# Kernel optimization log

Measured on AMD Instinct MI355X. Metric: run time of the kernel, lower is better.

Reference implementation:

```python
import jax, jax.numpy as jnp
import numpy as np

LOC_SIZE, CID_SIZE, UID_SIZE, TIM_SIZE = 10000, 300, 1000, 48
LOC_EMB, CID_EMB, UID_EMB, TIM_EMB = 256, 64, 64, 32
HID, ENC_HID = 500, 250            # hidden_size, history_hidden_size
SEQ, TGT = 2048, 256
INPUT = LOC_EMB + TIM_EMB + CID_EMB  # 352


def setup_inputs() -> dict:
    key = jax.random.key(0)
    ks = jax.random.split(key, 32)
    n = lambda i, shape, s=0.05: (jax.random.normal(ks[i], shape, dtype=jnp.float32) * s)
    d = {}
    d["loc"] = jax.random.randint(ks[0], (SEQ, 1), 0, LOC_SIZE)
    d["tim"] = jax.random.randint(ks[1], (SEQ, 1), 0, TIM_SIZE)
    d["cid"] = jax.random.randint(ks[2], (SEQ, 1), 0, CID_SIZE)
    d["uid"] = jax.random.randint(ks[3], (1,), 0, UID_SIZE)
    d["target"] = jax.random.randint(ks[4], (TGT, 1), 0, LOC_SIZE)
    d["target_len"] = TGT
    d["time_sim_matrix"] = jax.random.uniform(ks[5], (TIM_SIZE, TIM_SIZE), dtype=jnp.float32)
    # keep distances away from 0 since the model computes 1/dist
    d["poi_distance_matrix"] = jax.random.uniform(ks[6], (LOC_SIZE, LOC_SIZE), dtype=jnp.float32, minval=0.1, maxval=2.0)
    d["poi_cid_tim"] = jax.random.uniform(ks[7], (TIM_SIZE, CID_SIZE), dtype=jnp.float32)
    # embedding tables (emb_loc/emb_cid are pretrained+frozen in the original)
    d["weight"] = n(8, (LOC_SIZE, LOC_EMB))
    d["weight_cid"] = n(9, (CID_SIZE, CID_EMB))
    d["emb_uid_w"] = n(10, (UID_SIZE, UID_EMB))
    d["emb_tim_w"] = n(11, (TIM_SIZE, TIM_EMB))
    # bidirectional encoder LSTM (hidden 250), gate order i,f,g,o like torch
    d["enc_Wih_f"] = n(12, (4 * ENC_HID, INPUT))
    d["enc_Whh_f"] = n(13, (4 * ENC_HID, ENC_HID))
    d["enc_b_f"] = jnp.zeros((4 * ENC_HID,), jnp.float32)
    d["enc_Wih_b"] = n(14, (4 * ENC_HID, INPUT))
    d["enc_Whh_b"] = n(15, (4 * ENC_HID, ENC_HID))
    d["enc_b_b"] = jnp.zeros((4 * ENC_HID,), jnp.float32)
    # decoder LSTM (hidden 500)
    d["dec_Wih"] = n(16, (4 * HID, INPUT))
    d["dec_Whh"] = n(17, (4 * HID, HID))
    d["dec_b"] = jnp.zeros((4 * HID,), jnp.float32)
    # linear layers
    d["fc_user_w"] = n(18, (HID, UID_EMB))
    d["fc_user_b"] = jnp.zeros((HID,), jnp.float32)
    d["fc_final_w"] = n(19, (LOC_SIZE, 3 * HID))
    d["fc_final_b"] = jnp.zeros((LOC_SIZE,), jnp.float32)
    d["fc_final2_w"] = n(20, (HID, 3 * HID))
    d["fc_final2_b"] = jnp.zeros((HID,), jnp.float32)
    return d


def _lstm(x, Wih, Whh, b, H):
    """Single-layer LSTM, batch=1. x: [T, D] -> hs: [T, H]."""
    h0 = jnp.zeros((H,), x.dtype)
    c0 = jnp.zeros((H,), x.dtype)

    def step(carry, xt):
        h, c = carry
        z = Wih @ xt + Whh @ h + b
        i, f, g, o = jnp.split(z, 4)
        c = jax.nn.sigmoid(f) * c + jax.nn.sigmoid(i) * jnp.tanh(g)
        h = jax.nn.sigmoid(o) * jnp.tanh(c)
        return (h, c), h

    _, hs = jax.lax.scan(step, (h0, c0), x)
    return hs


def _table_attn(history, current, table, invert=False, causal=False):
    """Vectorized replacement for the nested-loop lookup attention.
    energies[i, j] = table[current[i], history[j]] (or its reciprocal),
    upper triangle left at 0 for the self-attn variants (as in the original),
    then softmax over the full row (torch F.softmax default dim=1 on 2D)."""
    e = table[current[:, None], history[None, :]]
    if invert:
        e = 1.0 / e
    if causal:
        nn_ = e.shape[0]
        e = jnp.where(jnp.tril(jnp.ones((nn_, nn_), bool)), e, jnp.zeros((), e.dtype))
    return jax.nn.softmax(e, axis=-1)


def reference(loc, tim, cid, uid, target, target_len,
              time_sim_matrix, poi_distance_matrix, poi_cid_tim,
              weight, weight_cid, emb_uid_w, emb_tim_w,
              enc_Wih_f, enc_Whh_f, enc_b_f, enc_Wih_b, enc_Whh_b, enc_b_b,
              dec_Wih, dec_Whh, dec_b,
              fc_user_w, fc_user_b, fc_final_w, fc_final_b, fc_final2_w, fc_final2_b):
    T = int(target_len)
    loc_f, tim_f, cid_f = loc[:, 0], tim[:, 0], cid[:, 0]

    # cross attention: current window attends to history via lookup tables
    attn_cid_time = _table_attn(cid_f[:-T], tim_f[-T:], poi_cid_tim)
    attn_loc = _table_attn(loc_f[:-T], loc_f[-T:], poi_distance_matrix, invert=True)
    attn_time = _table_attn(tim_f[:-T], tim_f[-T:], time_sim_matrix)
    # self attention on the current window (lower-triangular fill)
    self_cid_time = _table_attn(cid_f[-T:], tim_f[-T:], poi_cid_tim, causal=True)
    self_loc = _table_attn(loc_f[-T:], loc_f[-T:], poi_distance_matrix, invert=True, causal=True)
    self_time = _table_attn(tim_f[-T:], tim_f[-T:], time_sim_matrix, causal=True)

    # embeddings (dropout is identity in eval)
    x = jnp.concatenate([weight[loc_f], emb_tim_w[tim_f], weight_cid[cid_f]], axis=1)  # [SEQ, INPUT]
    hist_x, tgt_x = x[:-T], x[-T:]

    # bidirectional encoder over history
    hf = _lstm(hist_x, enc_Wih_f, enc_Whh_f, enc_b_f, ENC_HID)
    hb = _lstm(hist_x[::-1], enc_Wih_b, enc_Whh_b, enc_b_b, ENC_HID)[::-1]
    hidden_history = jnp.concatenate([hf, hb], axis=1)  # [SEQ-T, 2*ENC_HID=500]

    # decoder over current window
    hidden_state = _lstm(tgt_x, dec_Wih, dec_Whh, dec_b, HID)  # [T, 500]

    target_emb = weight[target[:, 0]]  # [T, LOC_EMB]

    uid_emb = emb_uid_w[uid] @ fc_user_w.T + fc_user_b  # [1, 500]
    user_attn = jax.nn.softmax(uid_emb @ hidden_history.T, axis=-1)  # [1, hist]
    context_user = user_attn @ hidden_history  # [1, 500]

    context = (attn_loc + attn_time + attn_cid_time) @ hidden_history  # [T, 500]
    hidden_state = (self_loc + self_time + self_cid_time) @ hidden_state  # [T, 500]

    hidden_state_all = hidden_state + uid_emb  # broadcast of repeat
    out = jnp.concatenate([hidden_state_all, context,
                           jnp.broadcast_to(context_user, (T, HID))], axis=1)  # [T, 1500]
    y = out @ fc_final_w.T + fc_final_b    # [T, LOC_SIZE]
    y1 = out @ fc_final2_w.T + fc_final2_b  # [T, HID]
    score = jax.nn.log_softmax(y, axis=-1)
    return score, y1, target_emb
```

## Files before the change

kernel.cpp:

```cpp
#include <hip/hip_runtime.h>
#include <stdint.h>

#define HIST 1792
#define TGT 256
#define SEQ 2048
#define INPUT 352
#define EHID 250
#define HID 500

typedef _Float16 h2_t __attribute__((ext_vector_type(2)));

static __device__ __forceinline__ float fdot2(uint32_t a, uint32_t b, float c) {
  return __builtin_amdgcn_fdot2(__builtin_bit_cast(h2_t, a),
                                __builtin_bit_cast(h2_t, b), c, false);
}
static __device__ __forceinline__ uint32_t packh2(float lo, float hi) {
  h2_t h; h[0] = (_Float16)lo; h[1] = (_Float16)hi;
  return __builtin_bit_cast(uint32_t, h);
}
static __device__ __forceinline__ uint4 packq(const float* p) {
  uint4 r;
  r.x = packh2(p[0], p[1]); r.y = packh2(p[2], p[3]);
  r.z = packh2(p[4], p[5]); r.w = packh2(p[6], p[7]);
  return r;
}
static __device__ __forceinline__ float dotq(uint4 w, uint4 h, float acc) {
  acc = fdot2(w.x, h.x, acc); acc = fdot2(w.y, h.y, acc);
  acc = fdot2(w.z, h.z, acc); acc = fdot2(w.w, h.w, acc);
  return acc;
}
static __device__ __forceinline__ float sigf(float x) {
  x = fminf(fmaxf(x, -30.f), 30.f);
  return 1.f / (1.f + __expf(-x));
}
static __device__ __forceinline__ float tanh_f(float x) {
  x = fminf(fmaxf(x, -15.f), 15.f);
  float e = __expf(2.f * x);
  return (e - 1.f) / (e + 1.f);
}

__global__ void k_embed(const int* __restrict__ loc, const int* __restrict__ tim,
                        const int* __restrict__ cid, const int* __restrict__ target,
                        const float* __restrict__ weight, const float* __restrict__ emb_tim_w,
                        const float* __restrict__ weight_cid,
                        float* __restrict__ x, float* __restrict__ te) {
  int t = blockIdx.x, tid = threadIdx.x;
  if (t < SEQ) {
    int l = loc[t], tm = tim[t], cd = cid[t];
    float* xr = x + (size_t)t * INPUT;
    for (int k = tid; k < 256; k += blockDim.x) xr[k] = weight[(size_t)l * 256 + k];
    for (int k = tid; k < 32; k += blockDim.x)  xr[256 + k] = emb_tim_w[tm * 32 + k];
    for (int k = tid; k < 64; k += blockDim.x)  xr[288 + k] = weight_cid[cd * 64 + k];
  } else {
    int i = t - SEQ;
    int tg = target[i];
    for (int k = tid; k < 256; k += blockDim.x) te[(size_t)i * 256 + k] = weight[(size_t)tg * 256 + k];
  }
}

__global__ void k_gemm_t(const float* __restrict__ A, int lda,
                         const float* __restrict__ W, const float* __restrict__ bias,
                         float* __restrict__ C, int ldc,
                         int M, int N, int K, int revA) {
  __shared__ float As[16][65];
  __shared__ float Ws[16][65];
  const int bn = blockIdx.x * 64, bm = blockIdx.y * 64;
  const int tid = threadIdx.x;
  const int tx = tid & 15, ty = tid >> 4;
  float acc[4][4] = {};
  for (int k0 = 0; k0 < K; k0 += 16) {
    for (int i = tid; i < 1024; i += 256) {
      int m = i >> 4, k = i & 15;
      int gm = bm + m, gk = k0 + k;
      float v = 0.f;
      if (gm < M && gk < K) { int am = revA ? (M - 1 - gm) : gm; v = A[(size_t)am * lda + gk]; }
      As[k][m] = v;
    }
    for (int i = tid; i < 1024; i += 256) {
      int n = i >> 4, k = i & 15;
      int gn = bn + n, gk = k0 + k;
      float v = 0.f;
      if (gn < N && gk < K) v = W[(size_t)gn * K + gk];
      Ws[k][n] = v;
    }
    __syncthreads();
#pragma unroll
    for (int k = 0; k < 16; k++) {
      float a0 = As[k][ty * 4 + 0], a1 = As[k][ty * 4 + 1], a2 = As[k][ty * 4 + 2], a3 = As[k][ty * 4 + 3];
      float b0 = Ws[k][tx * 4 + 0], b1 = Ws[k][tx * 4 + 1], b2 = Ws[k][tx * 4 + 2], b3 = Ws[k][tx * 4 + 3];
      acc[0][0] += a0 * b0; acc[0][1] += a0 * b1; acc[0][2] += a0 * b2; acc[0][3] += a0 * b3;
      acc[1][0] += a1 * b0; acc[1][1] += a1 * b1; acc[1][2] += a1 * b2; acc[1][3] += a1 * b3;
      acc[2][0] += a2 * b0; acc[2][1] += a2 * b1; acc[2][2] += a2 * b2; acc[2][3] += a2 * b3;
      acc[3][0] += a3 * b0; acc[3][1] += a3 * b1; acc[3][2] += a3 * b2; acc[3][3] += a3 * b3;
    }
    __syncthreads();
  }
  for (int i = 0; i < 4; i++) {
    int gm = bm + ty * 4 + i; if (gm >= M) continue;
    for (int j = 0; j < 4; j++) {
      int gn = bn + tx * 4 + j; if (gn >= N) continue;
      C[(size_t)gm * ldc + gn] = acc[i][j] + (bias ? bias[gn] : 0.f);
    }
  }
}

__global__ void k_gemm_nn(const float* __restrict__ A, int lda,
                          const float* __restrict__ B, int ldb,
                          const float* __restrict__ addvec,
                          float* __restrict__ C, int ldc,
                          int M, int N, int K) {
  __shared__ float As[16][65];
  __shared__ float Bs[16][65];
  const int bn = blockIdx.x * 64, bm = blockIdx.y * 64;
  const int tid = threadIdx.x;
  const int tx = tid & 15, ty = tid >> 4;
  float acc[4][4] = {};
  for (int k0 = 0; k0 < K; k0 += 16) {
    for (int i = tid; i < 1024; i += 256) {
      int m = i >> 4, k = i & 15;
      int gm = bm + m, gk = k0 + k;
      float v = 0.f;
      if (gm < M && gk < K) v = A[(size_t)gm * lda + gk];
      As[k][m] = v;
    }
    for (int i = tid; i < 1024; i += 256) {
      int k = i >> 6, n = i & 63;
      int gk = k0 + k, gn = bn + n;
      float v = 0.f;
      if (gk < K && gn < N) v = B[(size_t)gk * ldb + gn];
      Bs[k][n] = v;
    }
    __syncthreads();
#pragma unroll
    for (int k = 0; k < 16; k++) {
      float a0 = As[k][ty * 4 + 0], a1 = As[k][ty * 4 + 1], a2 = As[k][ty * 4 + 2], a3 = As[k][ty * 4 + 3];
      float b0 = Bs[k][tx * 4 + 0], b1 = Bs[k][tx * 4 + 1], b2 = Bs[k][tx * 4 + 2], b3 = Bs[k][tx * 4 + 3];
      acc[0][0] += a0 * b0; acc[0][1] += a0 * b1; acc[0][2] += a0 * b2; acc[0][3] += a0 * b3;
      acc[1][0] += a1 * b0; acc[1][1] += a1 * b1; acc[1][2] += a1 * b2; acc[1][3] += a1 * b3;
      acc[2][0] += a2 * b0; acc[2][1] += a2 * b1; acc[2][2] += a2 * b2; acc[2][3] += a2 * b3;
      acc[3][0] += a3 * b0; acc[3][1] += a3 * b1; acc[3][2] += a3 * b2; acc[3][3] += a3 * b3;
    }
    __syncthreads();
  }
  for (int i = 0; i < 4; i++) {
    int gm = bm + ty * 4 + i; if (gm >= M) continue;
    for (int j = 0; j < 4; j++) {
      int gn = bn + tx * 4 + j; if (gn >= N) continue;
      C[(size_t)gm * ldc + gn] = acc[i][j] + (addvec ? addvec[gn] : 0.f);
    }
  }
}

__launch_bounds__(512, 2)
__global__ void k_lstm(const float* __restrict__ A_f, const float* __restrict__ A_b,
                       const float* __restrict__ A_d,
                       const float* __restrict__ Whh_f, const float* __restrict__ Whh_b,
                       const float* __restrict__ Whh_d,
                       float* __restrict__ hh, float* __restrict__ hdec,
                       float* zpub, uint32_t* hpub, int* flag_z, int* flag_h) {
  const int b = blockIdx.x;
  const int tid = threadIdx.x;
  __shared__ uint4 h4e[32];
  __shared__ uint4 w4e[8][512];
  __shared__ float zbuf[1000];
  __shared__ uint4 h4d[64];
  __shared__ uint4 w4d[8][512];

  if (b < 2) {
    const float* A = (b == 0) ? A_f : A_b;
    const float* Whh = (b == 0) ? Whh_f : Whh_b;
    uint4 w0[28], w1[28];
    if (tid < 500) {
      const float* wr0 = Whh + (size_t)tid * EHID;
      const float* wr1 = Whh + (size_t)(tid + 500) * EHID;
      float tmp[32];
#pragma unroll
      for (int cc = 0; cc < 32; cc++) { int col = 224 + cc; tmp[cc] = (col < EHID) ? wr0[col] : 0.f; }
#pragma unroll
      for (int k = 0; k < 4; k++) w4e[k][tid] = packq(tmp + 8 * k);
#pragma unroll
      for (int cc = 0; cc < 32; cc++) { int col = 224 + cc; tmp[cc] = (col < EHID) ? wr1[col] : 0.f; }
#pragma unroll
      for (int k = 0; k < 4; k++) w4e[4 + k][tid] = packq(tmp + 8 * k);
#pragma unroll
      for (int q = 0; q < 28; q++) { w0[q] = packq(wr0 + 8 * q); w1[q] = packq(wr1 + 8 * q); }
    }
    if (tid < 32) h4e[tid] = make_uint4(0, 0, 0, 0);
    uint32_t* hde = (uint32_t*)h4e;
    float c = 0.f;
    __syncthreads();
    for (int t = 0; t < HIST; t++) {
      if (tid < 500) {
        float a0 = A[t * 1000 + tid];
        float a1 = A[t * 1000 + 500 + tid];
        float b0 = 0.f, b1 = 0.f;
#pragma unroll
        for (int q = 0; q < 28; q += 2) {
          uint4 h0 = h4e[q], h1 = h4e[q + 1];
          a0 = dotq(w0[q], h0, a0);
          a1 = dotq(w1[q], h0, a1);
          b0 = dotq(w0[q + 1], h1, b0);
          b1 = dotq(w1[q + 1], h1, b1);
        }
#pragma unroll
        for (int k = 0; k < 4; k += 2) {
          uint4 h0 = h4e[28 + k], h1 = h4e[29 + k];
          a0 = dotq(w4e[k][tid], h0, a0);
          a1 = dotq(w4e[4 + k][tid], h0, a1);
          b0 = dotq(w4e[k + 1][tid], h1, b0);
          b1 = dotq(w4e[5 + k][tid], h1, b1);
        }
        zbuf[tid] = a0 + b0;
        zbuf[500 + tid] = a1 + b1;
      }
      __syncthreads();
      float hval = 0.f;
      if (tid < EHID) {
        float zi = zbuf[tid], zf = zbuf[250 + tid], zg = zbuf[500 + tid], zo = zbuf[750 + tid];
        c = sigf(zf) * c + sigf(zi) * tanh_f(zg);
        hval = sigf(zo) * tanh_f(c);
        if (b == 0) hh[(size_t)t * HID + tid] = hval;
        else        hh[(size_t)(HIST - 1 - t) * HID + EHID + tid] = hval;
      }
      float hother = __shfl_xor(hval, 1);
      if (tid < EHID && !(tid & 1)) hde[tid >> 1] = packh2(hval, hother);
      __syncthreads();
    }
  } else {
    const int gi = b - 2;
    const int j = tid;
    const bool act = (j < 500);
    uint4 w[56];
    if (act) {
      const float* wr = Whh_d + (size_t)(gi * 500 + j) * HID;
      float tmp[64];
#pragma unroll
      for (int cc = 0; cc < 64; cc++) { int col = 448 + cc; tmp[cc] = (col < HID) ? wr[col] : 0.f; }
#pragma unroll
      for (int k = 0; k < 8; k++) w4d[k][tid] = packq(tmp + 8 * k);
#pragma unroll
      for (int q = 0; q < 56; q++) w[q] = packq(wr + 8 * q);
    }
    if (tid < 64) h4d[tid] = make_uint4(0, 0, 0, 0);
    uint32_t* hdd = (uint32_t*)h4d;
    float c = 0.f;
    __syncthreads();
    for (int t = 0; t < TGT; t++) {
      float z = 0.f;
      if (act) {
        float a0 = A_d[t * 2000 + gi * 500 + j];
        float a1 = 0.f, a2 = 0.f, a3 = 0.f;
#pragma unroll
        for (int q = 0; q < 56; q += 4) {
          uint4 h0 = h4d[q], h1 = h4d[q + 1], h2 = h4d[q + 2], h3 = h4d[q + 3];
          a0 = dotq(w[q], h0, a0);
          a1 = dotq(w[q + 1], h1, a1);
          a2 = dotq(w[q + 2], h2, a2);
          a3 = dotq(w[q + 3], h3, a3);
        }
#pragma unroll
        for (int k = 0; k < 8; k += 4) {
          uint4 h0 = h4d[56 + k], h1 = h4d[57 + k], h2 = h4d[58 + k], h3 = h4d[59 + k];
          a0 = dotq(w4d[k][tid], h0, a0);
          a1 = dotq(w4d[k + 1][tid], h1, a1);
          a2 = dotq(w4d[k + 2][tid], h2, a2);
          a3 = dotq(w4d[k + 3][tid], h3, a3);
        }
        z = (a0 + a1) + (a2 + a3);
      }
      if (gi < 3) {
        if (act) zpub[gi * 512 + j] = z;
        __threadfence();
        __syncthreads();
        if (tid == 0)
          __hip_atomic_store(&flag_z[t * 3 + gi], 1, __ATOMIC_RELEASE, __HIP_MEMORY_SCOPE_AGENT);
        if (tid == 0) {
          while (__hip_atomic_load(&flag_h[t], __ATOMIC_ACQUIRE, __HIP_MEMORY_SCOPE_AGENT) == 0)
            __builtin_amdgcn_s_sleep(2);
        }
        __syncthreads();
        if (tid < 250)
          hdd[tid] = __hip_atomic_load(&hpub[tid], __ATOMIC_RELAXED, __HIP_MEMORY_SCOPE_AGENT);
        __syncthreads();
      } else {
        if (tid == 0) {
          while (__hip_atomic_load(&flag_z[t * 3 + 0], __ATOMIC_ACQUIRE, __HIP_MEMORY_SCOPE_AGENT) == 0)
            __builtin_amdgcn_s_sleep(2);
          while (__hip_atomic_load(&flag_z[t * 3 + 1], __ATOMIC_ACQUIRE, __HIP_MEMORY_SCOPE_AGENT) == 0)
            __builtin_amdgcn_s_sleep(2);
          while (__hip_atomic_load(&flag_z[t * 3 + 2], __ATOMIC_ACQUIRE, __HIP_MEMORY_SCOPE_AGENT) == 0)
            __builtin_amdgcn_s_sleep(2);
        }
        __syncthreads();
        float hval = 0.f;
        if (act) {
          float zi = __hip_atomic_load(&zpub[0 * 512 + j], __ATOMIC_RELAXED, __HIP_MEMORY_SCOPE_AGENT);
          float zf = __hip_atomic_load(&zpub[1 * 512 + j], __ATOMIC_RELAXED, __HIP_MEMORY_SCOPE_AGENT);
          float zg = __hip_atomic_load(&zpub[2 * 512 + j], __ATOMIC_RELAXED, __HIP_MEMORY_SCOPE_AGENT);
          c = sigf(zf) * c + sigf(zi) * tanh_f(zg);
          hval = sigf(z) * tanh_f(c);
          hdec[(size_t)t * HID + j] = hval;
        }
        float hother = __shfl_xor(hval, 1);
        if (act && !(j & 1)) {
          uint32_t p = packh2(hval, hother);
          hdd[j >> 1] = p;
          hpub[j >> 1] = p;
        }
        __threadfence();
        __syncthreads();
        if (tid == 0)
          __hip_atomic_store(&flag_h[t], 1, __ATOMIC_RELEASE, __HIP_MEMORY_SCOPE_AGENT);
      }
    }
  }
}

__global__ void k_attn(const int* __restrict__ loc, const int* __restrict__ tim,
                       const int* __restrict__ cid,
                       const float* __restrict__ ts, const float* __restrict__ pd,
                       const float* __restrict__ pct,
                       float* __restrict__ S1, float* __restrict__ S2) {
  const int i = blockIdx.x;
  const int tid = threadIdx.x;
  __shared__ float e[HIST];
  __shared__ float red[256];
  const int loc_i = loc[HIST + i], tim_i = tim[HIST + i];
  for (int tab = 0; tab < 3; tab++) {
    for (int jj = tid; jj < HIST; jj += 256) {
      float v;
      if (tab == 0)      v = 1.f / pd[(size_t)loc_i * 10000 + loc[jj]];
      else if (tab == 1) v = ts[tim_i * 48 + tim[jj]];
      else               v = pct[tim_i * 300 + cid[jj]];
      e[jj] = v;
    }
    __syncthreads();
    float mx = -1e30f;
    for (int jj = tid; jj < HIST; jj += 256) mx = fmaxf(mx, e[jj]);
    red[tid] = mx; __syncthreads();
    for (int s = 128; s > 0; s >>= 1) { if (tid < s) red[tid] = fmaxf(red[tid], red[tid + s]); __syncthreads(); }
    mx = red[0]; __syncthreads();
    float sm = 0.f;
    for (int jj = tid; jj < HIST; jj += 256) sm += __expf(e[jj] - mx);
    red[tid] = sm; __syncthreads();
    for (int s = 128; s > 0; s >>= 1) { if (tid < s) red[tid] += red[tid + s]; __syncthreads(); }
    float inv = 1.f / red[0]; __syncthreads();
    for (int jj = tid; jj < HIST; jj += 256) {
      float p = __expf(e[jj] - mx) * inv;
      if (tab == 0) S1[(size_t)i * HIST + jj] = p; else S1[(size_t)i * HIST + jj] += p;
    }
    __syncthreads();
  }
  const int lj = loc[HIST + tid], tj = tim[HIST + tid], cj = cid[HIST + tid];
  for (int tab = 0; tab < 3; tab++) {
    float v;
    if (tab == 0)      v = 1.f / pd[(size_t)loc_i * 10000 + lj];
    else if (tab == 1) v = ts[tim_i * 48 + tj];
    else               v = pct[tim_i * 300 + cj];
    if (tid > i) v = 0.f;
    red[tid] = v; __syncthreads();
    for (int s = 128; s > 0; s >>= 1) { if (tid < s) red[tid] = fmaxf(red[tid], red[tid + s]); __syncthreads(); }
    float mx = red[0]; __syncthreads();
    float ex = __expf(v - mx);
    red[tid] = ex; __syncthreads();
    for (int s = 128; s > 0; s >>= 1) { if (tid < s) red[tid] += red[tid + s]; __syncthreads(); }
    float p = ex / red[0]; __syncthreads();
    if (tab == 0) S2[(size_t)i * TGT + tid] = p; else S2[(size_t)i * TGT + tid] += p;
    __syncthreads();
  }
}

__global__ void k_uid(const int* __restrict__ uid, const float* __restrict__ emb_uid_w,
                      const float* __restrict__ fc_user_w, const float* __restrict__ fc_user_b,
                      float* __restrict__ uid_emb) {
  const int tid = threadIdx.x;
  __shared__ float u[64];
  if (tid < 64) u[tid] = emb_uid_w[(size_t)uid[0] * 64 + tid];
  __syncthreads();
  if (tid < HID) {
    float a = fc_user_b[tid];
    for (int k = 0; k < 64; k++) a += u[k] * fc_user_w[tid * 64 + k];
    uid_emb[tid] = a;
  }
}

__global__ void k_user(const float* __restrict__ uid_emb, const float* __restrict__ hh,
                       float* __restrict__ out) {
  const int tid = threadIdx.x;
  __shared__ float s[HIST];
  __shared__ float red[1024];
  __shared__ float ue[HID];
  if (tid < HID) ue[tid] = uid_emb[tid];
  __syncthreads();
  for (int t = tid; t < HIST; t += 1024) {
    float a = 0.f;
    const float* hr = hh + (size_t)t * HID;
    for (int k = 0; k < HID; k++) a += ue[k] * hr[k];
    s[t] = a;
  }
  __syncthreads();
  float mx = -1e30f;
  for (int t = tid; t < HIST; t += 1024) mx = fmaxf(mx, s[t]);
  red[tid] = mx; __syncthreads();
  for (int st = 512; st > 0; st >>= 1) { if (tid < st) red[tid] = fmaxf(red[tid], red[tid + st]); __syncthreads(); }
  mx = red[0]; __syncthreads();
  float sm = 0.f;
  for (int t = tid; t < HIST; t += 1024) sm += __expf(s[t] - mx);
  red[tid] = sm; __syncthreads();
  for (int st = 512; st > 0; st >>= 1) { if (tid < st) red[tid] += red[tid + st]; __syncthreads(); }
  float inv = 1.f / red[0]; __syncthreads();
  for (int t = tid; t < HIST; t += 1024) s[t] = __expf(s[t] - mx) * inv;
  __syncthreads();
  if (tid < HID) {
    float a = 0.f;
    for (int t = 0; t < HIST; t++) a += s[t] * hh[(size_t)t * HID + tid];
    for (int i = 0; i < TGT; i++) out[(size_t)i * 1500 + 1000 + tid] = a;
  }
}

__global__ void k_logsoftmax(float* __restrict__ y) {
  const int i = blockIdx.x;
  const int tid = threadIdx.x;
  float* r = y + (size_t)i * 10000;
  __shared__ float red[1024];
  float mx = -1e30f;
  for (int j = tid; j < 10000; j += 1024) mx = fmaxf(mx, r[j]);
  red[tid] = mx; __syncthreads();
  for (int s = 512; s > 0; s >>= 1) { if (tid < s) red[tid] = fmaxf(red[tid], red[tid + s]); __syncthreads(); }
  mx = red[0]; __syncthreads();
  float sm = 0.f;
  for (int j = tid; j < 10000; j += 1024) sm += __expf(r[j] - mx);
  red[tid] = sm; __syncthreads();
  for (int s = 512; s > 0; s >>= 1) { if (tid < s) red[tid] += red[tid + s]; __syncthreads(); }
  float lse = mx + __logf(red[0]);
  __syncthreads();
  for (int j = tid; j < 10000; j += 1024) r[j] = r[j] - lse;
}

extern "C" void kernel_launch(void* const* d_in, const int* in_sizes, int n_in,
                              void* d_out, int out_size, void* d_ws, size_t ws_size,
                              hipStream_t stream) {
  (void)in_sizes; (void)n_in; (void)out_size; (void)ws_size;
  const int* loc = (const int*)d_in[0];
  const int* tim = (const int*)d_in[1];
  const int* cid = (const int*)d_in[2];
  const int* uid = (const int*)d_in[3];
  const int* target = (const int*)d_in[4];
  const float* ts = (const float*)d_in[6];
  const float* pd = (const float*)d_in[7];
  const float* pct = (const float*)d_in[8];
  const float* weight = (const float*)d_in[9];
  const float* weight_cid = (const float*)d_in[10];
  const float* emb_uid_w = (const float*)d_in[11];
  const float* emb_tim_w = (const float*)d_in[12];
  const float* enc_Wih_f = (const float*)d_in[13];
  const float* enc_Whh_f = (const float*)d_in[14];
  const float* enc_b_f = (const float*)d_in[15];
  const float* enc_Wih_b = (const float*)d_in[16];
  const float* enc_Whh_b = (const float*)d_in[17];
  const float* enc_b_b = (const float*)d_in[18];
  const float* dec_Wih = (const float*)d_in[19];
  const float* dec_Whh = (const float*)d_in[20];
  const float* dec_b = (const float*)d_in[21];
  const float* fc_user_w = (const float*)d_in[22];
  const float* fc_user_b = (const float*)d_in[23];
  const float* fc_final_w = (const float*)d_in[24];
  const float* fc_final_b = (const float*)d_in[25];
  const float* fc_final2_w = (const float*)d_in[26];
  const float* fc_final2_b = (const float*)d_in[27];

  float* score = (float*)d_out;
  float* y1 = score + (size_t)TGT * 10000;
  float* te = y1 + (size_t)TGT * HID;

  float* ws = (float*)d_ws;
  float* x = ws;
  float* A_f = x + (size_t)SEQ * INPUT;
  float* A_b = A_f + (size_t)HIST * 1000;
  float* A_d = A_b + (size_t)HIST * 1000;
  float* hh = A_d + (size_t)TGT * 2000;
  float* hdec = hh + (size_t)HIST * HID;
  float* S1 = hdec + (size_t)TGT * HID;
  float* S2 = S1 + (size_t)TGT * HIST;
  float* outb = S2 + (size_t)TGT * TGT;
  float* uid_emb = outb + (size_t)TGT * 1500;
  float* zpub = uid_emb + 512;
  uint32_t* hpub = (uint32_t*)(zpub + 3 * 512);
  int* flag_z = (int*)(hpub + 256);
  int* flag_h = flag_z + 3 * TGT;

  k_embed<<<dim3(SEQ + TGT), dim3(128), 0, stream>>>(loc, tim, cid, target, weight, emb_tim_w, weight_cid, x, te);

  k_gemm_t<<<dim3(16, 28), dim3(256), 0, stream>>>(x, INPUT, enc_Wih_f, enc_b_f, A_f, 1000, HIST, 1000, INPUT, 0);
  k_gemm_t<<<dim3(16, 28), dim3(256), 0, stream>>>(x, INPUT, enc_Wih_b, enc_b_b, A_b, 1000, HIST, 1000, INPUT, 1);
  k_gemm_t<<<dim3(32, 4), dim3(256), 0, stream>>>(x + (size_t)HIST * INPUT, INPUT, dec_Wih, dec_b, A_d, 2000, TGT, 2000, INPUT, 0);

  hipMemsetAsync(flag_z, 0, 4 * TGT * sizeof(int), stream);

  k_attn<<<dim3(TGT), dim3(256), 0, stream>>>(loc, tim, cid, ts, pd, pct, S1, S2);
  k_uid<<<dim3(1), dim3(512), 0, stream>>>(uid, emb_uid_w, fc_user_w, fc_user_b, uid_emb);

  k_lstm<<<dim3(6), dim3(512), 0, stream>>>(A_f, A_b, A_d, enc_Whh_f, enc_Whh_b, dec_Whh,
                                            hh, hdec, zpub, hpub, flag_z, flag_h);

  k_user<<<dim3(1), dim3(1024), 0, stream>>>(uid_emb, hh, outb);
  k_gemm_nn<<<dim3(8, 4), dim3(256), 0, stream>>>(S2, TGT, hdec, HID, uid_emb, outb, 1500, TGT, HID, TGT);
  k_gemm_nn<<<dim3(8, 4), dim3(256), 0, stream>>>(S1, HIST, hh, HID, nullptr, outb + 500, 1500, TGT, HID, HIST);

  k_gemm_t<<<dim3(157, 4), dim3(256), 0, stream>>>(outb, 1500, fc_final_w, fc_final_b, score, 10000, TGT, 10000, 1500, 0);
  k_gemm_t<<<dim3(8, 4), dim3(256), 0, stream>>>(outb, 1500, fc_final2_w, fc_final2_b, y1, 500, TGT, 500, 1500, 0);

  k_logsoftmax<<<dim3(TGT), dim3(1024), 0, stream>>>(score);
}
```

Before: 5.403 ms.

## Split LSTM recurrent weights across VGPRs, AGPRs and LDS at one block per CU

The recurrent weight slices in the LSTM kernel are now spread over three places: part in regular VGPRs, part in LDS (a much larger shared buffer), and part in accumulation registers (AGPRs) written and read with inline asm. Launch bounds drop the two-blocks-per-CU requirement, which frees the full register file and LDS for one block. The aim is to keep every weight on chip without spilling and to cut per-step shared-memory traffic on the serial recurrence. The cost is extra accvgpr read instructions each step and lower occupancy. The hpub store is also made an explicit atomic.

New measurement: 6.371 ms. +17.9%, slower.

```diff
diff --git a/kernel.cpp b/kernel.cpp
--- a/kernel.cpp
+++ b/kernel.cpp
@@ -38,6 +38,8 @@
   float e = __expf(2.f * x);
   return (e - 1.f) / (e + 1.f);
 }
+#define AW(dst, src) asm volatile("v_accvgpr_write_b32 %0, %1" : "=a"(dst) : "v"(src))
+#define AR(dst, src) asm volatile("v_accvgpr_read_b32 %0, %1" : "=v"(dst) : "a"(src))
 
 __global__ void k_embed(const int* __restrict__ loc, const int* __restrict__ tim,
                         const int* __restrict__ cid, const int* __restrict__ target,
@@ -151,7 +153,8 @@
   }
 }
 
-__launch_bounds__(512, 2)
+#define WBYTES (18 * 512 * 16)
+__launch_bounds__(512)
 __global__ void k_lstm(const float* __restrict__ A_f, const float* __restrict__ A_b,
                        const float* __restrict__ A_d,
                        const float* __restrict__ Whh_f, const float* __restrict__ Whh_b,
@@ -160,55 +163,73 @@
                        float* zpub, uint32_t* hpub, int* flag_z, int* flag_h) {
   const int b = blockIdx.x;
   const int tid = threadIdx.x;
-  __shared__ uint4 h4e[32];
-  __shared__ uint4 w4e[8][512];
-  __shared__ float zbuf[1000];
-  __shared__ uint4 h4d[64];
-  __shared__ uint4 w4d[8][512];
+  __shared__ __align__(16) unsigned char smem[WBYTES + 5120];
+  uint4* wls = (uint4*)smem;
 
   if (b < 2) {
+    uint4* h4e = (uint4*)(smem + WBYTES);
+    float* zbuf = (float*)(smem + WBYTES + 512);
     const float* A = (b == 0) ? A_f : A_b;
     const float* Whh = (b == 0) ? Whh_f : Whh_b;
-    uint4 w0[28], w1[28];
-    if (tid < 500) {
+    const bool act = tid < 500;
+    uint4 w0[12], w1[12];
+    uint32_t wa[88];
+    if (act) {
       const float* wr0 = Whh + (size_t)tid * EHID;
       const float* wr1 = Whh + (size_t)(tid + 500) * EHID;
-      float tmp[32];
-#pragma unroll
-      for (int cc = 0; cc < 32; cc++) { int col = 224 + cc; tmp[cc] = (col < EHID) ? wr0[col] : 0.f; }
-#pragma unroll
-      for (int k = 0; k < 4; k++) w4e[k][tid] = packq(tmp + 8 * k);
-#pragma unroll
-      for (int cc = 0; cc < 32; cc++) { int col = 224 + cc; tmp[cc] = (col < EHID) ? wr1[col] : 0.f; }
-#pragma unroll
-      for (int k = 0; k < 4; k++) w4e[4 + k][tid] = packq(tmp + 8 * k);
-#pragma unroll
-      for (int q = 0; q < 28; q++) { w0[q] = packq(wr0 + 8 * q); w1[q] = packq(wr1 + 8 * q); }
+#pragma unroll
+      for (int q = 12; q <= 20; q++) {
+        wls[((q - 12) * 2 + 0) * 512 + tid] = packq(wr0 + 8 * q);
+        wls[((q - 12) * 2 + 1) * 512 + tid] = packq(wr1 + 8 * q);
+      }
+#pragma unroll
+      for (int r = 0; r < 2; r++) {
+        const float* wr = r ? wr1 : wr0;
+#pragma unroll
+        for (int q = 21; q <= 31; q++) {
+          float tmp[8];
+#pragma unroll
+          for (int cc = 0; cc < 8; cc++) { int col = 8 * q + cc; tmp[cc] = (col < EHID) ? wr[col] : 0.f; }
+          uint4 pq = packq(tmp);
+          int base = (r * 11 + (q - 21)) * 4;
+          AW(wa[base + 0], pq.x); AW(wa[base + 1], pq.y);
+          AW(wa[base + 2], pq.z); AW(wa[base + 3], pq.w);
+        }
+      }
+#pragma unroll
+      for (int q = 0; q < 12; q++) { w0[q] = packq(wr0 + 8 * q); w1[q] = packq(wr1 + 8 * q); }
     }
     if (tid < 32) h4e[tid] = make_uint4(0, 0, 0, 0);
     uint32_t* hde = (uint32_t*)h4e;
     float c = 0.f;
     __syncthreads();
     for (int t = 0; t < HIST; t++) {
-      if (tid < 500) {
+      if (act) {
         float a0 = A[t * 1000 + tid];
         float a1 = A[t * 1000 + 500 + tid];
         float b0 = 0.f, b1 = 0.f;
 #pragma unroll
-        for (int q = 0; q < 28; q += 2) {
+        for (int q = 0; q < 12; q += 2) {
           uint4 h0 = h4e[q], h1 = h4e[q + 1];
-          a0 = dotq(w0[q], h0, a0);
-          a1 = dotq(w1[q], h0, a1);
-          b0 = dotq(w0[q + 1], h1, b0);
-          b1 = dotq(w1[q + 1], h1, b1);
-        }
-#pragma unroll
-        for (int k = 0; k < 4; k += 2) {
-          uint4 h0 = h4e[28 + k], h1 = h4e[29 + k];
-          a0 = dotq(w4e[k][tid], h0, a0);
-          a1 = dotq(w4e[4 + k][tid], h0, a1);
-          b0 = dotq(w4e[k + 1][tid], h1, b0);
-          b1 = dotq(w4e[5 + k][tid], h1, b1);
+          a0 = dotq(w0[q], h0, a0);     a1 = dotq(w1[q], h0, a1);
+          b0 = dotq(w0[q + 1], h1, b0); b1 = dotq(w1[q + 1], h1, b1);
+        }
+#pragma unroll
+        for (int q = 0; q < 9; q++) {
+          uint4 hq = h4e[12 + q];
+          a0 = dotq(wls[(2 * q) * 512 + tid], hq, a0);
+          a1 = dotq(wls[(2 * q + 1) * 512 + tid], hq, a1);
+        }
+#pragma unroll
+        for (int k = 0; k < 11; k++) {
+          uint4 hq = h4e[21 + k];
+          uint4 u0, u1;
+          AR(u0.x, wa[k * 4 + 0]); AR(u0.y, wa[k * 4 + 1]);
+          AR(u0.z, wa[k * 4 + 2]); AR(u0.w, wa[k * 4 + 3]);
+          AR(u1.x, wa[(11 + k) * 4 + 0]); AR(u1.y, wa[(11 + k) * 4 + 1]);
+          AR(u1.z, wa[(11 + k) * 4 + 2]); AR(u1.w, wa[(11 + k) * 4 + 3]);
+          b0 = dotq(u0, hq, b0);
+          b1 = dotq(u1, hq, b1);
         }
         zbuf[tid] = a0 + b0;
         zbuf[500 + tid] = a1 + b1;
@@ -227,19 +248,28 @@
       __syncthreads();
     }
   } else {
+    uint4* h4d = (uint4*)(smem + WBYTES);
     const int gi = b - 2;
     const int j = tid;
     const bool act = (j < 500);
-    uint4 w[56];
+    uint4 w[24];
+    uint32_t wa[88];
     if (act) {
       const float* wr = Whh_d + (size_t)(gi * 500 + j) * HID;
-      float tmp[64];
-#pragma unroll
-      for (int cc = 0; cc < 64; cc++) { int col = 448 + cc; tmp[cc] = (col < HID) ? wr[col] : 0.f; }
-#pragma unroll
-      for (int k = 0; k < 8; k++) w4d[k][tid] = packq(tmp + 8 * k);
-#pragma unroll
-      for (int q = 0; q < 56; q++) w[q] = packq(wr + 8 * q);
+#pragma unroll
+      for (int q = 24; q <= 41; q++) wls[(q - 24) * 512 + tid] = packq(wr + 8 * q);
+#pragma unroll
+      for (int q = 42; q <= 63; q++) {
+        float tmp[8];
+#pragma unroll
+        for (int cc = 0; cc < 8; cc++) { int col = 8 * q + cc; tmp[cc] = (col < HID) ? wr[col] : 0.f; }
+        uint4 pq = packq(tmp);
+        int base = (q - 42) * 4;
+        AW(wa[base + 0], pq.x); AW(wa[base + 1], pq.y);
+        AW(wa[base + 2], pq.z); AW(wa[base + 3], pq.w);
+      }
+#pragma unroll
+      for (int q = 0; q < 24; q++) w[q] = packq(wr + 8 * q);
     }
     if (tid < 64) h4d[tid] = make_uint4(0, 0, 0, 0);
     uint32_t* hdd = (uint32_t*)h4d;
@@ -251,20 +281,24 @@
         float a0 = A_d[t * 2000 + gi * 500 + j];
         float a1 = 0.f, a2 = 0.f, a3 = 0.f;
 #pragma unroll
-        for (int q = 0; q < 56; q += 4) {
-          uint4 h0 = h4d[q], h1 = h4d[q + 1], h2 = h4d[q + 2], h3 = h4d[q + 3];
-          a0 = dotq(w[q], h0, a0);
-          a1 = dotq(w[q + 1], h1, a1);
-          a2 = dotq(w[q + 2], h2, a2);
-          a3 = dotq(w[q + 3], h3, a3);
-        }
-#pragma unroll
-        for (int k = 0; k < 8; k += 4) {
-          uint4 h0 = h4d[56 + k], h1 = h4d[57 + k], h2 = h4d[58 + k], h3 = h4d[59 + k];
-          a0 = dotq(w4d[k][tid], h0, a0);
-          a1 = dotq(w4d[k + 1][tid], h1, a1);
-          a2 = dotq(w4d[k + 2][tid], h2, a2);
-          a3 = dotq(w4d[k + 3][tid], h3, a3);
+        for (int q = 0; q < 24; q += 4) {
+          a0 = dotq(w[q], h4d[q], a0);
+          a1 = dotq(w[q + 1], h4d[q + 1], a1);
+          a2 = dotq(w[q + 2], h4d[q + 2], a2);
+          a3 = dotq(w[q + 3], h4d[q + 3], a3);
+        }
+#pragma unroll
+        for (int q = 0; q < 18; q += 2) {
+          a0 = dotq(wls[q * 512 + tid], h4d[24 + q], a0);
+          a1 = dotq(wls[(q + 1) * 512 + tid], h4d[25 + q], a1);
+        }
+#pragma unroll
+        for (int k = 0; k < 22; k++) {
+          uint4 hq = h4d[42 + k];
+          uint4 u;
+          AR(u.x, wa[k * 4 + 0]); AR(u.y, wa[k * 4 + 1]);
+          AR(u.z, wa[k * 4 + 2]); AR(u.w, wa[k * 4 + 3]);
+          a2 = dotq(u, hq, a2);
         }
         z = (a0 + a1) + (a2 + a3);
       }
@@ -305,7 +339,7 @@
         if (act && !(j & 1)) {
           uint32_t p = packh2(hval, hother);
           hdd[j >> 1] = p;
-          hpub[j >> 1] = p;
+          __hip_atomic_store(&hpub[j >> 1], p, __ATOMIC_RELAXED, __HIP_MEMORY_SCOPE_AGENT);
         }
         __threadfence();
         __syncthreads();
```
